# Performance work log

Measured on AMD Instinct MI355X. Metric: run time of the kernel, lower is better.

## Reference

```python
import jax, jax.numpy as jnp
import numpy as np

GROUP_SIZE = 128

def setup_inputs() -> dict:
    key = jax.random.key(0)
    k1, k2, k3, k4 = jax.random.split(key, 4)
    in_f, out_f = 4096, 4096
    num_groups = (in_f + GROUP_SIZE - 1) // GROUP_SIZE  # 32
    x = jax.random.normal(k1, (4, 2048, in_f), dtype=jnp.float32)
    qweight = jax.random.randint(k2, (out_f, in_f), 0, 16, dtype=jnp.int32)
    scales = jax.random.uniform(k3, (out_f, num_groups), dtype=jnp.float32)
    bias = jax.random.normal(k4, (out_f,), dtype=jnp.float32)
    return {"x": x, "qweight": qweight, "scales": scales, "bias": bias}

def reference(x, qweight, scales, bias):
    out_f, in_f = qweight.shape
    # group-wise dequantize: broadcast each per-group scale over its columns
    scale_full = jnp.repeat(scales, GROUP_SIZE, axis=1)[:, :in_f]  # [out, in]
    weight = qweight.astype(scales.dtype) * scale_full             # [out, in]
    # F.linear(x, weight, bias) == x @ weight.T + bias
    return jnp.einsum('bsi,oi->bso', x, weight) + bias
```

## Files before the change

### kernel.cpp

```cpp
#include <hip/hip_runtime.h>
#include <hip/hip_bf16.h>

typedef __bf16 bf16_t;
typedef __bf16 bf16x8 __attribute__((ext_vector_type(8)));
typedef float  f32x4  __attribute__((ext_vector_type(4)));
typedef int    i32x4  __attribute__((ext_vector_type(4)));

static constexpr int M_ = 8192;
static constexpr int N_ = 4096;
static constexpr int K_ = 4096;

static constexpr int BM = 256, BN = 256, BK = 64;
static constexpr int NT = K_ / BK;
static constexpr int HT_ELEMS  = 128 * 64;
static constexpr int BUF_ELEMS = 2 * HT_ELEMS;

__device__ __forceinline__ void load_lds16(const bf16_t* g, bf16_t* l) {
  __builtin_amdgcn_global_load_lds(
      (const __attribute__((address_space(1))) void*)g,
      (__attribute__((address_space(3))) void*)l,
      16, 0, 0);
}

#define MFMA16(a, b, c) __builtin_amdgcn_mfma_f32_16x16x32_bf16((a), (b), (c), 0, 0, 0)

__global__ __launch_bounds__(256) void cvt_x_kernel(const float* __restrict__ x,
                                                    bf16_t* __restrict__ xb) {
  const size_t i = ((size_t)blockIdx.x * 256 + threadIdx.x) * 8;
  const f32x4 f0 = __builtin_nontemporal_load((const f32x4*)(x + i));
  const f32x4 f1 = __builtin_nontemporal_load((const f32x4*)(x + i + 4));
  bf16x8 o;
  o[0] = (bf16_t)f0[0]; o[1] = (bf16_t)f0[1]; o[2] = (bf16_t)f0[2]; o[3] = (bf16_t)f0[3];
  o[4] = (bf16_t)f1[0]; o[5] = (bf16_t)f1[1]; o[6] = (bf16_t)f1[2]; o[7] = (bf16_t)f1[3];
  *(bf16x8*)(xb + i) = o;
}

__global__ __launch_bounds__(256) void dequant_kernel(const int* __restrict__ q,
                                                      const float* __restrict__ s,
                                                      bf16_t* __restrict__ wb) {
  const size_t base = ((size_t)blockIdx.x * 256 + threadIdx.x) * 8;
  const int o  = (int)(base >> 12);
  const int ii = (int)(base & 4095);
  const float sc = s[(o << 5) + (ii >> 7)];
  const i32x4 q0 = __builtin_nontemporal_load((const i32x4*)(q + base));
  const i32x4 q1 = __builtin_nontemporal_load((const i32x4*)(q + base + 4));
  bf16x8 w;
  w[0] = (bf16_t)((float)q0[0] * sc); w[1] = (bf16_t)((float)q0[1] * sc);
  w[2] = (bf16_t)((float)q0[2] * sc); w[3] = (bf16_t)((float)q0[3] * sc);
  w[4] = (bf16_t)((float)q1[0] * sc); w[5] = (bf16_t)((float)q1[1] * sc);
  w[6] = (bf16_t)((float)q1[2] * sc); w[7] = (bf16_t)((float)q1[3] * sc);
  *(bf16x8*)(wb + base) = w;
}

__global__ __launch_bounds__(512, 2) void gemm_kernel(const bf16_t* __restrict__ A,
                                                      const bf16_t* __restrict__ B,
                                                      const float* __restrict__ bias,
                                                      float* __restrict__ C) {
  __shared__ __align__(16) bf16_t As[2 * BUF_ELEMS];
  __shared__ __align__(16) bf16_t Bs[2 * BUF_ELEMS];

  const int tid  = threadIdx.x;
  const int lane = tid & 63;
  const int wave = tid >> 6;
  const int ln = lane & 15;
  const int lq = lane >> 4;
  const int wm = wave >> 2;
  const int wn = wave & 3;

  const int bid = blockIdx.x;
  const int wg  = (bid & 7) * 64 + (bid >> 3);
  const int bn  = (wg & 15) * BN;
  const int bm  = (wg >> 4) * BM;

  const int r_sub = tid >> 3;
  const int g_col = ((tid & 7) ^ (r_sub & 7)) * 8;
  const size_t a_base = (size_t)(bm + r_sub) * K_ + g_col;
  const size_t b_base = (size_t)(bn + r_sub) * K_ + g_col;
  const int lds_off = tid * 8;

  auto stageA = [&](int t, int h) {
    bf16_t* d = As + (t & 1) * BUF_ELEMS + h * HT_ELEMS + lds_off;
    const bf16_t* s = A + a_base + (size_t)(h * 128) * K_ + (size_t)t * BK;
    load_lds16(s, d);
    load_lds16(s + (size_t)64 * K_, d + 4096);
  };
  auto stageB = [&](int t, int h) {
    bf16_t* d = Bs + (t & 1) * BUF_ELEMS + h * HT_ELEMS + lds_off;
    const bf16_t* s = B + b_base + (size_t)(h * 128) * K_ + (size_t)t * BK;
    load_lds16(s, d);
    load_lds16(s + (size_t)64 * K_, d + 4096);
  };

  const int kx0 = (lq * 8) ^ ((ln & 7) * 8);
  const int kx1 = (32 + lq * 8) ^ ((ln & 7) * 8);
  const int a_row_off = (wm * 16 + ln) * 64;
  const int b_row_off = (wn * 32 + ln) * 64;

  f32x4 acc[8][4] = {};

  stageA(0, 0); stageB(0, 0); stageB(0, 1); stageA(0, 1);
  stageA(1, 0); stageB(1, 0); stageB(1, 1);
  asm volatile("s_waitcnt vmcnt(6)" ::: "memory");
  __builtin_amdgcn_s_barrier();

  for (int T = 0; T < NT; ++T) {
    const bf16_t* as = As + (T & 1) * BUF_ELEMS;
    const bf16_t* bs = Bs + (T & 1) * BUF_ELEMS;
    bf16x8 af[4][2], bqA[2][2], bqB[2][2];

#pragma unroll
    for (int i = 0; i < 4; ++i) {
      const bf16_t* p = as + a_row_off + i * 2048;
      af[i][0] = *(const bf16x8*)(p + kx0);
      af[i][1] = *(const bf16x8*)(p + kx1);
    }
#pragma unroll
    for (int j = 0; j < 2; ++j) {
      const bf16_t* p = bs + b_row_off + j * 1024;
      bqA[j][0] = *(const bf16x8*)(p + kx0);
      bqA[j][1] = *(const bf16x8*)(p + kx1);
    }
    if (T + 1 < NT) stageA(T + 1, 1);
    __builtin_amdgcn_s_barrier();
    __builtin_amdgcn_s_setprio(1);
#pragma unroll
    for (int i = 0; i < 4; ++i)
#pragma unroll
      for (int j = 0; j < 2; ++j) {
        acc[i][j] = MFMA16(af[i][0], bqA[j][0], acc[i][j]);
        acc[i][j] = MFMA16(af[i][1], bqA[j][1], acc[i][j]);
      }
    __builtin_amdgcn_s_setprio(0);
    asm volatile("s_waitcnt lgkmcnt(0)" ::: "memory");
    __builtin_amdgcn_s_barrier();

#pragma unroll
    for (int j = 0; j < 2; ++j) {
      const bf16_t* p = bs + HT_ELEMS + b_row_off + j * 1024;
      bqB[j][0] = *(const bf16x8*)(p + kx0);
      bqB[j][1] = *(const bf16x8*)(p + kx1);
    }
    if (T + 2 < NT) stageA(T + 2, 0);
    __builtin_amdgcn_s_barrier();
    __builtin_amdgcn_s_setprio(1);
#pragma unroll
    for (int i = 0; i < 4; ++i)
#pragma unroll
      for (int j = 0; j < 2; ++j) {
        acc[i][j + 2] = MFMA16(af[i][0], bqB[j][0], acc[i][j + 2]);
        acc[i][j + 2] = MFMA16(af[i][1], bqB[j][1], acc[i][j + 2]);
      }
    __builtin_amdgcn_s_setprio(0);
    asm volatile("s_waitcnt lgkmcnt(0)" ::: "memory");
    __builtin_amdgcn_s_barrier();

#pragma unroll
    for (int i = 0; i < 4; ++i) {
      const bf16_t* p = as + HT_ELEMS + a_row_off + i * 2048;
      af[i][0] = *(const bf16x8*)(p + kx0);
      af[i][1] = *(const bf16x8*)(p + kx1);
    }
    if (T + 2 < NT) stageB(T + 2, 0);
    __builtin_amdgcn_s_barrier();
    __builtin_amdgcn_s_setprio(1);
#pragma unroll
    for (int i = 0; i < 4; ++i)
#pragma unroll
      for (int j = 0; j < 2; ++j) {
        acc[i + 4][j + 2] = MFMA16(af[i][0], bqB[j][0], acc[i + 4][j + 2]);
        acc[i + 4][j + 2] = MFMA16(af[i][1], bqB[j][1], acc[i + 4][j + 2]);
      }
    __builtin_amdgcn_s_setprio(0);
    asm volatile("s_waitcnt lgkmcnt(0)" ::: "memory");
    __builtin_amdgcn_s_barrier();

    if (T + 2 < NT) {
      stageB(T + 2, 1);
      asm volatile("s_waitcnt vmcnt(6)" ::: "memory");
    } else {
      asm volatile("s_waitcnt vmcnt(0)" ::: "memory");
    }
    __builtin_amdgcn_s_barrier();
    __builtin_amdgcn_sched_barrier(0);
    __builtin_amdgcn_s_setprio(1);
#pragma unroll
    for (int i = 0; i < 4; ++i)
#pragma unroll
      for (int j = 0; j < 2; ++j) {
        acc[i + 4][j] = MFMA16(af[i][0], bqA[j][0], acc[i + 4][j]);
        acc[i + 4][j] = MFMA16(af[i][1], bqA[j][1], acc[i + 4][j]);
      }
    __builtin_amdgcn_s_setprio(0);
    __builtin_amdgcn_s_barrier();
  }

#pragma unroll
  for (int j = 0; j < 4; ++j) {
    const int col = bn + (j >> 1) * 128 + wn * 32 + (j & 1) * 16 + ln;
    const float bv = bias[col];
#pragma unroll
    for (int i = 0; i < 8; ++i) {
      const int row0 = bm + (i >> 2) * 128 + (i & 3) * 32 + wm * 16 + lq * 4;
      float* cp = C + (size_t)row0 * N_ + col;
#pragma unroll
      for (int r = 0; r < 4; ++r) {
        __builtin_nontemporal_store(acc[i][j][r] + bv, cp);
        cp += N_;
      }
    }
  }
}

extern "C" void kernel_launch(void* const* d_in, const int* in_sizes, int n_in,
                              void* d_out, int out_size, void* d_ws, size_t ws_size,
                              hipStream_t stream) {
  const float* x    = (const float*)d_in[0];
  const int*   qw   = (const int*)d_in[1];
  const float* sc   = (const float*)d_in[2];
  const float* bias = (const float*)d_in[3];
  float* out = (float*)d_out;

  bf16_t* xb = (bf16_t*)d_ws;
  bf16_t* wb = xb + (size_t)M_ * K_;

  cvt_x_kernel<<<(int)(((size_t)M_ * K_) / (256 * 8)), 256, 0, stream>>>(x, xb);
  dequant_kernel<<<(int)(((size_t)N_ * K_) / (256 * 8)), 256, 0, stream>>>(qw, sc, wb);

  const int nwg = (N_ / BN) * (M_ / BM);
  gemm_kernel<<<nwg, 512, 0, stream>>>(xb, wb, bias, out);
}
```

Baseline: 479.7 us.

## Enlarge GEMM tile to 256x512 with BK=32 and per-wave 128x128 outputs

Reshapes the GEMM main loop to a 256x512 workgroup tile with a K step of 32, so each wave owns a 128x128 output block held in 64 MFMA accumulators. The loop becomes four MFMA quadrants per K step, each fed by one set of LDS fragment loads, and it uses a new XOR swizzle for 32-wide rows. The workgroup-to-tile grid swizzle is dropped. The aim is more operand reuse per LDS read and fewer global loads per FLOP. The cost is doubled accumulator register pressure under the same launch bounds, which risks spills or lower occupancy, and the grid now has only 256 workgroups.

Result: slower. 1.436 ms (+199.3%).

```diff
diff --git a/kernel.cpp b/kernel.cpp
--- a/kernel.cpp
+++ b/kernel.cpp
@@ -10,10 +10,10 @@
 static constexpr int N_ = 4096;
 static constexpr int K_ = 4096;
 
-static constexpr int BM = 256, BN = 256, BK = 64;
+static constexpr int BM = 256, BN = 512, BK = 32;
 static constexpr int NT = K_ / BK;
-static constexpr int HT_ELEMS  = 128 * 64;
-static constexpr int BUF_ELEMS = 2 * HT_ELEMS;
+static constexpr int A_ELEMS = BM * BK;
+static constexpr int B_ELEMS = BN * BK;
 
 __device__ __forceinline__ void load_lds16(const bf16_t* g, bf16_t* l) {
   __builtin_amdgcn_global_load_lds(
@@ -56,8 +56,8 @@
                                                       const bf16_t* __restrict__ B,
                                                       const float* __restrict__ bias,
                                                       float* __restrict__ C) {
-  __shared__ __align__(16) bf16_t As[2 * BUF_ELEMS];
-  __shared__ __align__(16) bf16_t Bs[2 * BUF_ELEMS];
+  __shared__ __align__(16) bf16_t As[2 * A_ELEMS];
+  __shared__ __align__(16) bf16_t Bs[2 * B_ELEMS];
 
   const int tid  = threadIdx.x;
   const int lane = tid & 63;
@@ -68,139 +68,111 @@
   const int wn = wave & 3;
 
   const int bid = blockIdx.x;
-  const int wg  = (bid & 7) * 64 + (bid >> 3);
-  const int bn  = (wg & 15) * BN;
-  const int bm  = (wg >> 4) * BM;
-
-  const int r_sub = tid >> 3;
-  const int g_col = ((tid & 7) ^ (r_sub & 7)) * 8;
+  const int bn  = (bid & 7) * BN;
+  const int bm  = (bid >> 3) * BM;
+
+  const int r_sub  = tid >> 2;
+  const int swz_r  = ((tid >> 2) & 3) ^ ((tid >> 4) & 3);
+  const int g_col  = (((tid & 3) ^ swz_r) * 8);
   const size_t a_base = (size_t)(bm + r_sub) * K_ + g_col;
   const size_t b_base = (size_t)(bn + r_sub) * K_ + g_col;
   const int lds_off = tid * 8;
 
-  auto stageA = [&](int t, int h) {
-    bf16_t* d = As + (t & 1) * BUF_ELEMS + h * HT_ELEMS + lds_off;
-    const bf16_t* s = A + a_base + (size_t)(h * 128) * K_ + (size_t)t * BK;
-    load_lds16(s, d);
-    load_lds16(s + (size_t)64 * K_, d + 4096);
+  auto stageA = [&](int t) {
+#pragma unroll
+    for (int c = 0; c < 2; ++c)
+      load_lds16(A + a_base + (size_t)c * 128 * K_ + (size_t)t * BK,
+                 As + (t & 1) * A_ELEMS + c * 4096 + lds_off);
   };
-  auto stageB = [&](int t, int h) {
-    bf16_t* d = Bs + (t & 1) * BUF_ELEMS + h * HT_ELEMS + lds_off;
-    const bf16_t* s = B + b_base + (size_t)(h * 128) * K_ + (size_t)t * BK;
-    load_lds16(s, d);
-    load_lds16(s + (size_t)64 * K_, d + 4096);
+  auto stageB = [&](int t) {
+#pragma unroll
+    for (int c = 0; c < 4; ++c)
+      load_lds16(B + b_base + (size_t)c * 128 * K_ + (size_t)t * BK,
+                 Bs + (t & 1) * B_ELEMS + c * 4096 + lds_off);
   };
 
-  const int kx0 = (lq * 8) ^ ((ln & 7) * 8);
-  const int kx1 = (32 + lq * 8) ^ ((ln & 7) * 8);
-  const int a_row_off = (wm * 16 + ln) * 64;
-  const int b_row_off = (wn * 32 + ln) * 64;
-
-  f32x4 acc[8][4] = {};
-
-  stageA(0, 0); stageB(0, 0); stageB(0, 1); stageA(0, 1);
-  stageA(1, 0); stageB(1, 0); stageB(1, 1);
+  const int kx = ((lq ^ (ln & 3) ^ ((ln >> 2) & 3)) * 8);
+  const int a_row = (wm * 128 + ln) * BK + kx;
+  const int b_row = (wn * 128 + ln) * BK + kx;
+
+  f32x4 acc[8][8] = {};
+
+  stageB(0); stageA(0); stageB(1); stageA(1);
   asm volatile("s_waitcnt vmcnt(6)" ::: "memory");
   __builtin_amdgcn_s_barrier();
 
   for (int T = 0; T < NT; ++T) {
-    const bf16_t* as = As + (T & 1) * BUF_ELEMS;
-    const bf16_t* bs = Bs + (T & 1) * BUF_ELEMS;
-    bf16x8 af[4][2], bqA[2][2], bqB[2][2];
-
-#pragma unroll
-    for (int i = 0; i < 4; ++i) {
-      const bf16_t* p = as + a_row_off + i * 2048;
-      af[i][0] = *(const bf16x8*)(p + kx0);
-      af[i][1] = *(const bf16x8*)(p + kx1);
-    }
-#pragma unroll
-    for (int j = 0; j < 2; ++j) {
-      const bf16_t* p = bs + b_row_off + j * 1024;
-      bqA[j][0] = *(const bf16x8*)(p + kx0);
-      bqA[j][1] = *(const bf16x8*)(p + kx1);
-    }
-    if (T + 1 < NT) stageA(T + 1, 1);
-    __builtin_amdgcn_s_barrier();
+    const bf16_t* as = As + (T & 1) * A_ELEMS;
+    const bf16_t* bs = Bs + (T & 1) * B_ELEMS;
+    bf16x8 af[8], bq[8];
+
+    af[0] = *(const bf16x8*)(as + a_row);
+#pragma unroll
+    for (int j = 0; j < 4; ++j)
+      bq[j] = *(const bf16x8*)(bs + b_row + j * 512);
+#pragma unroll
+    for (int i = 1; i < 4; ++i)
+      af[i] = *(const bf16x8*)(as + a_row + i * 512);
     __builtin_amdgcn_s_setprio(1);
 #pragma unroll
     for (int i = 0; i < 4; ++i)
 #pragma unroll
-      for (int j = 0; j < 2; ++j) {
-        acc[i][j] = MFMA16(af[i][0], bqA[j][0], acc[i][j]);
-        acc[i][j] = MFMA16(af[i][1], bqA[j][1], acc[i][j]);
-      }
+      for (int j = 0; j < 4; ++j)
+        acc[i][j] = MFMA16(af[i], bq[j], acc[i][j]);
     __builtin_amdgcn_s_setprio(0);
     asm volatile("s_waitcnt lgkmcnt(0)" ::: "memory");
     __builtin_amdgcn_s_barrier();
 
 #pragma unroll
-    for (int j = 0; j < 2; ++j) {
-      const bf16_t* p = bs + HT_ELEMS + b_row_off + j * 1024;
-      bqB[j][0] = *(const bf16x8*)(p + kx0);
-      bqB[j][1] = *(const bf16x8*)(p + kx1);
-    }
-    if (T + 2 < NT) stageA(T + 2, 0);
-    __builtin_amdgcn_s_barrier();
+    for (int j = 4; j < 8; ++j)
+      bq[j] = *(const bf16x8*)(bs + b_row + j * 512);
     __builtin_amdgcn_s_setprio(1);
 #pragma unroll
     for (int i = 0; i < 4; ++i)
 #pragma unroll
-      for (int j = 0; j < 2; ++j) {
-        acc[i][j + 2] = MFMA16(af[i][0], bqB[j][0], acc[i][j + 2]);
-        acc[i][j + 2] = MFMA16(af[i][1], bqB[j][1], acc[i][j + 2]);
-      }
+      for (int j = 4; j < 8; ++j)
+        acc[i][j] = MFMA16(af[i], bq[j], acc[i][j]);
     __builtin_amdgcn_s_setprio(0);
     asm volatile("s_waitcnt lgkmcnt(0)" ::: "memory");
     __builtin_amdgcn_s_barrier();
 
 #pragma unroll
-    for (int i = 0; i < 4; ++i) {
-      const bf16_t* p = as + HT_ELEMS + a_row_off + i * 2048;
-      af[i][0] = *(const bf16x8*)(p + kx0);
-      af[i][1] = *(const bf16x8*)(p + kx1);
-    }
-    if (T + 2 < NT) stageB(T + 2, 0);
-    __builtin_amdgcn_s_barrier();
-    __builtin_amdgcn_s_setprio(1);
-#pragma unroll
-    for (int i = 0; i < 4; ++i)
-#pragma unroll
-      for (int j = 0; j < 2; ++j) {
-        acc[i + 4][j + 2] = MFMA16(af[i][0], bqB[j][0], acc[i + 4][j + 2]);
-        acc[i + 4][j + 2] = MFMA16(af[i][1], bqB[j][1], acc[i + 4][j + 2]);
-      }
+    for (int i = 4; i < 8; ++i)
+      af[i] = *(const bf16x8*)(as + a_row + i * 512);
+    if (T + 2 < NT) stageB(T + 2);
+    __builtin_amdgcn_s_setprio(1);
+#pragma unroll
+    for (int i = 4; i < 8; ++i)
+#pragma unroll
+      for (int j = 4; j < 8; ++j)
+        acc[i][j] = MFMA16(af[i], bq[j], acc[i][j]);
     __builtin_amdgcn_s_setprio(0);
     asm volatile("s_waitcnt lgkmcnt(0)" ::: "memory");
     __builtin_amdgcn_s_barrier();
 
+    if (T + 2 < NT) stageA(T + 2);
+    __builtin_amdgcn_s_setprio(1);
+#pragma unroll
+    for (int i = 4; i < 8; ++i)
+#pragma unroll
+      for (int j = 0; j < 4; ++j)
+        acc[i][j] = MFMA16(af[i], bq[j], acc[i][j]);
+    __builtin_amdgcn_s_setprio(0);
     if (T + 2 < NT) {
-      stageB(T + 2, 1);
       asm volatile("s_waitcnt vmcnt(6)" ::: "memory");
     } else {
       asm volatile("s_waitcnt vmcnt(0)" ::: "memory");
     }
     __builtin_amdgcn_s_barrier();
-    __builtin_amdgcn_sched_barrier(0);
-    __builtin_amdgcn_s_setprio(1);
-#pragma unroll
-    for (int i = 0; i < 4; ++i)
-#pragma unroll
-      for (int j = 0; j < 2; ++j) {
-        acc[i + 4][j] = MFMA16(af[i][0], bqA[j][0], acc[i + 4][j]);
-        acc[i + 4][j] = MFMA16(af[i][1], bqA[j][1], acc[i + 4][j]);
-      }
-    __builtin_amdgcn_s_setprio(0);
-    __builtin_amdgcn_s_barrier();
   }
 
 #pragma unroll
-  for (int j = 0; j < 4; ++j) {
-    const int col = bn + (j >> 1) * 128 + wn * 32 + (j & 1) * 16 + ln;
+  for (int j = 0; j < 8; ++j) {
+    const int col = bn + wn * 128 + j * 16 + ln;
     const float bv = bias[col];
 #pragma unroll
     for (int i = 0; i < 8; ++i) {
-      const int row0 = bm + (i >> 2) * 128 + (i & 3) * 32 + wm * 16 + lq * 4;
+      const int row0 = bm + wm * 128 + i * 16 + lq * 4;
       float* cp = C + (size_t)row0 * N_ + col;
 #pragma unroll
       for (int r = 0; r < 4; ++r) {
@@ -226,6 +198,6 @@
   cvt_x_kernel<<<(int)(((size_t)M_ * K_) / (256 * 8)), 256, 0, stream>>>(x, xb);
   dequant_kernel<<<(int)(((size_t)N_ * K_) / (256 * 8)), 256, 0, stream>>>(qw, sc, wb);
 
-  const int nwg = (N_ / BN) * (M_ / BM);
+  const int nwg = (M_ / BM) * (N_ / BN);
   gemm_kernel<<<nwg, 512, 0, stream>>>(xb, wb, bias, out);
 }
```
